# Optimization experiments

Hardware: AMD Instinct MI355X
Metric: run time of the kernel (lower is better)

## Reference

```python
import jax, jax.numpy as jnp
import numpy as np

IN_U = 1024
OUT_U = 1024
BATCH = 4096
HID = 20            # ceil(log2(IN_U*OUT_U)), layer_encoding_dim=0 since num_layers=1
MLP_H = 10
FEAT = 3 + 3 * HID  # 63


def setup_inputs() -> dict:
    key = jax.random.key(0)
    ks = jax.random.split(key, 6)
    X = jax.random.normal(ks[0], (BATCH, IN_U), dtype=jnp.float32)
    weight = jax.random.normal(ks[1], (IN_U, OUT_U), dtype=jnp.float32) * 0.02
    # binary positional encodings per cell (encode_weight_hidden_states)
    k = jnp.arange(IN_U * OUT_U, dtype=jnp.int32).reshape(IN_U, OUT_U)
    shifts = jnp.arange(HID - 1, -1, -1, dtype=jnp.int32)
    hidden = ((k[..., None] >> shifts) & 1).astype(jnp.float32)  # [IN_U, OUT_U, HID]
    W1 = jax.random.normal(ks[2], (FEAT, MLP_H), dtype=jnp.float32) / np.float32(np.sqrt(FEAT))
    b1 = jnp.zeros((MLP_H,), jnp.float32)
    W2 = jax.random.normal(ks[3], (MLP_H, MLP_H), dtype=jnp.float32) / np.float32(np.sqrt(MLP_H))
    b2 = jnp.zeros((MLP_H,), jnp.float32)
    W3 = jax.random.normal(ks[4], (MLP_H, 1 + HID), dtype=jnp.float32) / np.float32(np.sqrt(MLP_H))
    b3 = jnp.zeros((1 + HID,), jnp.float32)
    return {"X": X, "weight": weight, "hidden": hidden,
            "W1": W1, "b1": b1, "W2": W2, "b2": b2, "W3": W3, "b3": b3}


def reference(X, weight, hidden, W1, b1, W2, b2, W3, b3):
    n, m = weight.shape
    # exclude-self column means ('forward') and row means ('backward')
    fwd_mean = (jnp.sum(weight, axis=0, keepdims=True) - weight) / (n - 1)   # [n,m]
    bwd_mean = (jnp.sum(weight, axis=1, keepdims=True) - weight) / (m - 1)   # [n,m]
    fwd_hs = (jnp.sum(hidden, axis=0, keepdims=True) - hidden) / (n - 1)     # [n,m,H]
    bwd_hs = (jnp.sum(hidden, axis=1, keepdims=True) - hidden) / (m - 1)     # [n,m,H]
    feat = jnp.concatenate(
        [weight[..., None], fwd_mean[..., None], bwd_mean[..., None],
         hidden, fwd_hs, bwd_hs], axis=-1)                                   # [n,m,3+3H]
    h = jax.nn.relu(jnp.einsum('nmf,fh->nmh', feat, W1) + b1)
    h = jax.nn.relu(jnp.einsum('nmh,hk->nmk', h, W2) + b2)
    updates = jnp.einsum('nmk,ko->nmo', h, W3) + b3                          # [n,m,1+H]
    new_weight = weight + updates[..., 0]
    # (hidden states also get updates[...,1:] in the torch module, but only the
    #  softmax output is returned)
    logits = jax.nn.relu(X @ new_weight)                                     # [B,m]
    return jax.nn.softmax(logits, axis=-1)
```

## Files before the change

### kernel.cpp

```cpp
#include <hip/hip_runtime.h>
#include <hip/hip_bf16.h>
#include <stdint.h>


#define RS_OFF      0
#define CSPART_OFF  4096
#define BT_OFF      266240
#define AH_OFF      2363392
#define CH_OFF      10752000

typedef __attribute__((ext_vector_type(8))) _Float16 f16x8;
typedef __attribute__((ext_vector_type(4))) float f32x4;

__device__ __forceinline__ unsigned short f2h(float x) {
    _Float16 h = (_Float16)x;
    unsigned short u;
    __builtin_memcpy(&u, &h, 2);
    return u;
}
__device__ __forceinline__ float h2f(unsigned short u) {
    _Float16 h;
    __builtin_memcpy(&h, &u, 2);
    return (float)h;
}
__device__ __forceinline__ void gld16(const void* g, void* l) {
    __builtin_amdgcn_global_load_lds(
        (const __attribute__((address_space(1))) unsigned*)g,
        (__attribute__((address_space(3))) unsigned*)l, 16, 0, 0);
}

__global__ __launch_bounds__(256) void k_pre(const float* __restrict__ w,
        float* __restrict__ rs, float* __restrict__ cs_part) {
    __shared__ float part[4][1024];
    int t = threadIdx.x;
    int lane = t & 63, wv = t >> 6;
    int r0 = blockIdx.x * 16 + wv * 4;
    float ccol[16];
    #pragma unroll
    for (int j = 0; j < 16; ++j) ccol[j] = 0.f;
    #pragma unroll
    for (int rr = 0; rr < 4; ++rr) {
        int row = r0 + rr;
        float rsum = 0.f;
        #pragma unroll
        for (int j = 0; j < 16; ++j) {
            float v = w[(size_t)row * 1024 + j * 64 + lane];
            ccol[j] += v;
            rsum += v;
        }
        #pragma unroll
        for (int o = 32; o; o >>= 1) rsum += __shfl_down(rsum, o);
        if (lane == 0) rs[row] = rsum;
    }
    #pragma unroll
    for (int j = 0; j < 16; ++j) part[wv][j * 64 + lane] = ccol[j];
    __syncthreads();
    #pragma unroll
    for (int j = 0; j < 4; ++j) {
        int c = t + j * 256;
        cs_part[(size_t)blockIdx.x * 1024 + c] =
            part[0][c] + part[1][c] + part[2][c] + part[3][c];
    }
}

__global__ __launch_bounds__(256) void k_nw(const float* __restrict__ w,
        const float* __restrict__ X,
        const float* __restrict__ rs, const float* __restrict__ cs_part,
        const float* __restrict__ W1, const float* __restrict__ b1,
        const float* __restrict__ W2, const float* __restrict__ b2,
        const float* __restrict__ W3, const float* __restrict__ b3,
        unsigned short* __restrict__ Bt, unsigned short* __restrict__ Ah) {
    __shared__ float sW1[630], sW2[100], sb1[10], sb2[10], sw3[10], sa[10];
    __shared__ float rs_loc[32], cs_loc[32];
    __shared__ float rn_loc[320], cm_loc[320];
    __shared__ float st[32][33];
    int t = threadIdx.x;
    if (blockIdx.x >= 1024) {
        int b2x = blockIdx.x - 1024;
        int rb = (b2x & 7) * 512 + (b2x >> 3) * 4;
        size_t rbase = (size_t)rb * 1024;
        #pragma unroll
        for (int p = 0; p < 4; ++p) {
            size_t idx = rbase + p * 1024 + t * 4;
            float4 v = *(const float4*)&X[idx];
            ushort4 h;
            h.x = f2h(v.x); h.y = f2h(v.y); h.z = f2h(v.z); h.w = f2h(v.w);
            *(ushort4*)&Ah[idx] = h;
        }
        return;
    }
    int n0 = (blockIdx.x & 31) * 32;
    int m0 = (blockIdx.x >> 5) * 32;
    const float inv = 1.0f / 1023.0f;

    for (int i = t; i < 630; i += 256) sW1[i] = W1[i];
    if (t < 100) sW2[t] = W2[t];
    if (t >= 128 && t < 138) { sb1[t - 128] = b1[t - 128]; sb2[t - 128] = b2[t - 128]; }
    if (t >= 160 && t < 170) sw3[t - 160] = W3[(t - 160) * 21];
    if (t >= 192 && t < 224) rs_loc[t - 192] = rs[n0 + t - 192];
    if (t >= 224 && t < 256) {
        float s = 0.f;
        #pragma unroll
        for (int p = 0; p < 64; ++p) s += cs_part[(size_t)p * 1024 + m0 + (t - 224)];
        cs_loc[t - 224] = s;
    }
    float b30 = b3[0];
    __syncthreads();
    if (t < 10) sa[t] = sW1[t] - (sW1[10 + t] + sW1[20 + t]) * inv;
    for (int id = t; id < 640; id += 256) {
        int h = id % 10, i = (id / 10) & 31, side = id >= 320;
        if (!side) {
            int n = n0 + i;
            float v = rs_loc[i] * sW1[20 + h] * inv;
            #pragma unroll
            for (int j = 0; j < 10; j++) {
                float bit = (float)((n >> (9 - j)) & 1);
                v += bit * (sW1[(3 + j) * 10 + h] + sW1[(43 + j) * 10 + h]
                            - sW1[(23 + j) * 10 + h] * inv);
                v += (512.0f * inv) * sW1[(23 + j) * 10 + h];
            }
            rn_loc[i * 10 + h] = v;
        } else {
            int m = m0 + i;
            float v = cs_loc[i] * sW1[10 + h] * inv + sb1[h];
            #pragma unroll
            for (int j = 0; j < 10; j++) {
                float bit = (float)((m >> (9 - j)) & 1);
                v += bit * (sW1[(13 + j) * 10 + h] + sW1[(33 + j) * 10 + h]
                            - sW1[(53 + j) * 10 + h] * inv);
                v += (512.0f * inv) * sW1[(53 + j) * 10 + h];
            }
            cm_loc[i * 10 + h] = v;
        }
    }
    __syncthreads();
    int ml = t & 31;
    #pragma unroll
    for (int i = 0; i < 4; i++) {
        int nl = (t >> 5) + 8 * i;
        float wv = w[(size_t)(n0 + nl) * 1024 + m0 + ml];
        float h1[10];
        #pragma unroll
        for (int h = 0; h < 10; h++)
            h1[h] = fmaxf(wv * sa[h] + rn_loc[nl * 10 + h] + cm_loc[ml * 10 + h], 0.f);
        float u = b30;
        #pragma unroll
        for (int k = 0; k < 10; k++) {
            float h2 = sb2[k];
            #pragma unroll
            for (int h = 0; h < 10; h++) h2 += h1[h] * sW2[h * 10 + k];
            u += fmaxf(h2, 0.f) * sw3[k];
        }
        st[nl][ml] = wv + u;
    }
    __syncthreads();
    int mrow = t >> 3, kc = t & 7;
    unsigned short hi4[4];
    #pragma unroll
    for (int j = 0; j < 4; j++)
        hi4[j] = f2h(st[kc * 4 + j][mrow]);
    size_t base = (size_t)(m0 + mrow) * 1024 + n0 + kc * 4;
    *(ushort4*)&Bt[base] = make_ushort4(hi4[0], hi4[1], hi4[2], hi4[3]);
}

__global__ __launch_bounds__(256, 3) void k_gemm13(const unsigned short* __restrict__ Ah,
        const unsigned short* __restrict__ Bt, unsigned short* __restrict__ Ch) {
    __shared__ unsigned short sAh[128 * 64];
    __shared__ unsigned short sBh[64 * 64];
    int tid = threadIdx.x;
    int lane = tid & 63, w = tid >> 6;
    int b = blockIdx.x;
    int xcd = b & 7, s = b >> 3;
    int ty = (xcd << 2) | (s >> 4);
    int tx = s & 15;
    int n0 = tx * 64, m0 = ty * 128;
    int wm = (w >> 1) * 64, wn = (w & 1) * 32;
    int quad = lane >> 4, l16 = lane & 15;

    f32x4 acc[4][2];
    #pragma unroll
    for (int i = 0; i < 4; i++)
        #pragma unroll
        for (int j = 0; j < 2; j++) acc[i][j] = (f32x4)0.f;

    for (int it = 0; it < 16; ++it) {
        int kb = it * 64;
        __syncthreads();
        #pragma unroll
        for (int s2 = 0; s2 < 4; ++s2) {
            int P = s2 * 256 + tid;
            int row = P >> 3;
            int seg = (P & 7) ^ (row & 7);
            int ldsOff = (s2 * 256 + w * 64) * 8;
            size_t ga = (size_t)(m0 + row) * 1024 + kb + seg * 8;
            gld16(&Ah[ga], &sAh[ldsOff]);
        }
        #pragma unroll
        for (int s2 = 0; s2 < 2; ++s2) {
            int P = s2 * 256 + tid;
            int row = P >> 3;
            int seg = (P & 7) ^ (row & 7);
            int ldsOff = (s2 * 256 + w * 64) * 8;
            size_t gb = (size_t)(n0 + row) * 1024 + kb + seg * 8;
            gld16(&Bt[gb], &sBh[ldsOff]);
        }
        __syncthreads();
        #pragma unroll
        for (int ks = 0; ks < 2; ++ks) {
            int segk = ks * 4 + quad;
            f16x8 ah[4], bh[2];
            #pragma unroll
            for (int i = 0; i < 4; ++i) {
                int ra = wm + i * 16 + l16;
                int ca = (ra * 8 + (segk ^ (ra & 7))) * 8;
                ah[i] = *(const f16x8*)&sAh[ca];
            }
            #pragma unroll
            for (int j = 0; j < 2; ++j) {
                int rb = wn + j * 16 + l16;
                int cb = (rb * 8 + (segk ^ (rb & 7))) * 8;
                bh[j] = *(const f16x8*)&sBh[cb];
            }
            #pragma unroll
            for (int i = 0; i < 4; ++i)
                #pragma unroll
                for (int j = 0; j < 2; ++j)
                    acc[i][j] = __builtin_amdgcn_mfma_f32_16x16x32_f16(ah[i], bh[j], acc[i][j], 0, 0, 0);
        }
    }
    #pragma unroll
    for (int i = 0; i < 4; ++i) {
        int mr = m0 + wm + i * 16 + quad * 4;
        #pragma unroll
        for (int j = 0; j < 2; ++j) {
            int nc = n0 + wn + j * 16 + l16;
            #pragma unroll
            for (int r = 0; r < 4; ++r)
                Ch[(size_t)(mr + r) * 1024 + nc] = f2h(fmaxf(acc[i][j][r], 0.f));
        }
    }
}

__global__ __launch_bounds__(256) void k_softmax3(const unsigned short* __restrict__ Ch,
        float* __restrict__ out) {
    int b = blockIdx.x;
    int row = (b & 7) * 512 + (b >> 3);
    int t = threadIdx.x, lane = t & 63, wv = t >> 6;
    __shared__ float red[8];
    ushort4 hv = *(const ushort4*)&Ch[(size_t)row * 1024 + t * 4];
    float4 v;
    v.x = h2f(hv.x); v.y = h2f(hv.y); v.z = h2f(hv.z); v.w = h2f(hv.w);
    float lm = fmaxf(fmaxf(v.x, v.y), fmaxf(v.z, v.w));
    #pragma unroll
    for (int o = 32; o; o >>= 1) lm = fmaxf(lm, __shfl_down(lm, o));
    if (lane == 0) red[wv] = lm;
    __syncthreads();
    float mx = fmaxf(fmaxf(red[0], red[1]), fmaxf(red[2], red[3]));
    float4 e;
    e.x = __expf(v.x - mx); e.y = __expf(v.y - mx);
    e.z = __expf(v.z - mx); e.w = __expf(v.w - mx);
    float ls = e.x + e.y + e.z + e.w;
    #pragma unroll
    for (int o = 32; o; o >>= 1) ls += __shfl_down(ls, o);
    if (lane == 0) red[4 + wv] = ls;
    __syncthreads();
    float inv = 1.0f / (red[4] + red[5] + red[6] + red[7]);
    e.x *= inv; e.y *= inv; e.z *= inv; e.w *= inv;
    *(float4*)&out[(size_t)row * 1024 + t * 4] = e;
}

extern "C" void kernel_launch(void* const* d_in, const int* in_sizes, int n_in,
                              void* d_out, int out_size, void* d_ws, size_t ws_size,
                              hipStream_t stream) {
    const float* X  = (const float*)d_in[0];
    const float* W  = (const float*)d_in[1];
    const float* W1 = (const float*)d_in[3];
    const float* b1 = (const float*)d_in[4];
    const float* W2 = (const float*)d_in[5];
    const float* b2 = (const float*)d_in[6];
    const float* W3 = (const float*)d_in[7];
    const float* b3 = (const float*)d_in[8];

    char* wsb = (char*)d_ws;
    float* rs            = (float*)(wsb + RS_OFF);
    float* cs_part       = (float*)(wsb + CSPART_OFF);
    unsigned short* Bt   = (unsigned short*)(wsb + BT_OFF);
    unsigned short* Ah   = (unsigned short*)(wsb + AH_OFF);
    unsigned short* Ch   = (unsigned short*)(wsb + CH_OFF);
    float* out = (float*)d_out;

    k_pre<<<64, 256, 0, stream>>>(W, rs, cs_part);
    k_nw<<<2048, 256, 0, stream>>>(W, X, rs, cs_part, W1, b1, W2, b2, W3, b3, Bt, Ah);
    k_gemm13<<<512, 256, 0, stream>>>(Ah, Bt, Ch);
    k_softmax3<<<4096, 256, 0, stream>>>(Ch, out);
}
```

Before: 175.1 us.

## Fuse X fp32-to-fp16 conversion into GEMM with register prefetch

Removes the separate conversion pass that wrote a half-precision copy of X to workspace inside k_nw. The GEMM now reads fp32 X directly, converts it in registers and stores it to LDS, with a register prefetch of the next K tile to overlap the global loads. This avoids writing and rereading an 8 MB intermediate. In exchange the A loads become synchronous register loads of twice the bytes, re-read by each of the 16 column-tile blocks, and register pressure rises under the 3-waves launch bound.

```diff
diff --git a/kernel.cpp b/kernel.cpp
--- a/kernel.cpp
+++ b/kernel.cpp
@@ -6,7 +6,6 @@
 #define RS_OFF      0
 #define CSPART_OFF  4096
 #define BT_OFF      266240
-#define AH_OFF      2363392
 #define CH_OFF      10752000
 
 typedef __attribute__((ext_vector_type(8))) _Float16 f16x8;
@@ -64,31 +63,16 @@
 }
 
 __global__ __launch_bounds__(256) void k_nw(const float* __restrict__ w,
-        const float* __restrict__ X,
         const float* __restrict__ rs, const float* __restrict__ cs_part,
         const float* __restrict__ W1, const float* __restrict__ b1,
         const float* __restrict__ W2, const float* __restrict__ b2,
         const float* __restrict__ W3, const float* __restrict__ b3,
-        unsigned short* __restrict__ Bt, unsigned short* __restrict__ Ah) {
+        unsigned short* __restrict__ Bt) {
     __shared__ float sW1[630], sW2[100], sb1[10], sb2[10], sw3[10], sa[10];
     __shared__ float rs_loc[32], cs_loc[32];
     __shared__ float rn_loc[320], cm_loc[320];
     __shared__ float st[32][33];
     int t = threadIdx.x;
-    if (blockIdx.x >= 1024) {
-        int b2x = blockIdx.x - 1024;
-        int rb = (b2x & 7) * 512 + (b2x >> 3) * 4;
-        size_t rbase = (size_t)rb * 1024;
-        #pragma unroll
-        for (int p = 0; p < 4; ++p) {
-            size_t idx = rbase + p * 1024 + t * 4;
-            float4 v = *(const float4*)&X[idx];
-            ushort4 h;
-            h.x = f2h(v.x); h.y = f2h(v.y); h.z = f2h(v.z); h.w = f2h(v.w);
-            *(ushort4*)&Ah[idx] = h;
-        }
-        return;
-    }
     int n0 = (blockIdx.x & 31) * 32;
     int m0 = (blockIdx.x >> 5) * 32;
     const float inv = 1.0f / 1023.0f;
@@ -163,7 +147,7 @@
     *(ushort4*)&Bt[base] = make_ushort4(hi4[0], hi4[1], hi4[2], hi4[3]);
 }
 
-__global__ __launch_bounds__(256, 3) void k_gemm13(const unsigned short* __restrict__ Ah,
+__global__ __launch_bounds__(256, 3) void k_gemm14(const float* __restrict__ X,
         const unsigned short* __restrict__ Bt, unsigned short* __restrict__ Ch) {
     __shared__ unsigned short sAh[128 * 64];
     __shared__ unsigned short sBh[64 * 64];
@@ -183,17 +167,35 @@
         #pragma unroll
         for (int j = 0; j < 2; j++) acc[i][j] = (f32x4)0.f;
 
+    int rowA[4], segA[4];
+    #pragma unroll
+    for (int s2 = 0; s2 < 4; ++s2) {
+        int P = s2 * 256 + tid;
+        rowA[s2] = P >> 3;
+        segA[s2] = (P & 7) ^ (rowA[s2] & 7);
+    }
+
+    float4 pf0[4], pf1[4];
+    #pragma unroll
+    for (int s2 = 0; s2 < 4; ++s2) {
+        const float* ga = &X[(size_t)(m0 + rowA[s2]) * 1024 + segA[s2] * 8];
+        pf0[s2] = *(const float4*)(ga);
+        pf1[s2] = *(const float4*)(ga + 4);
+    }
+
     for (int it = 0; it < 16; ++it) {
         int kb = it * 64;
         __syncthreads();
         #pragma unroll
         for (int s2 = 0; s2 < 4; ++s2) {
             int P = s2 * 256 + tid;
-            int row = P >> 3;
-            int seg = (P & 7) ^ (row & 7);
-            int ldsOff = (s2 * 256 + w * 64) * 8;
-            size_t ga = (size_t)(m0 + row) * 1024 + kb + seg * 8;
-            gld16(&Ah[ga], &sAh[ldsOff]);
+            float4 a0 = pf0[s2], a1 = pf1[s2];
+            f16x8 hv;
+            hv[0] = (_Float16)a0.x; hv[1] = (_Float16)a0.y;
+            hv[2] = (_Float16)a0.z; hv[3] = (_Float16)a0.w;
+            hv[4] = (_Float16)a1.x; hv[5] = (_Float16)a1.y;
+            hv[6] = (_Float16)a1.z; hv[7] = (_Float16)a1.w;
+            *(f16x8*)&sAh[P * 8] = hv;
         }
         #pragma unroll
         for (int s2 = 0; s2 < 2; ++s2) {
@@ -203,6 +205,15 @@
             int ldsOff = (s2 * 256 + w * 64) * 8;
             size_t gb = (size_t)(n0 + row) * 1024 + kb + seg * 8;
             gld16(&Bt[gb], &sBh[ldsOff]);
+        }
+        if (it < 15) {
+            int kb2 = kb + 64;
+            #pragma unroll
+            for (int s2 = 0; s2 < 4; ++s2) {
+                const float* ga = &X[(size_t)(m0 + rowA[s2]) * 1024 + kb2 + segA[s2] * 8];
+                pf0[s2] = *(const float4*)(ga);
+                pf1[s2] = *(const float4*)(ga + 4);
+            }
         }
         __syncthreads();
         #pragma unroll
@@ -285,12 +296,11 @@
     float* rs            = (float*)(wsb + RS_OFF);
     float* cs_part       = (float*)(wsb + CSPART_OFF);
     unsigned short* Bt   = (unsigned short*)(wsb + BT_OFF);
-    unsigned short* Ah   = (unsigned short*)(wsb + AH_OFF);
     unsigned short* Ch   = (unsigned short*)(wsb + CH_OFF);
     float* out = (float*)d_out;
 
     k_pre<<<64, 256, 0, stream>>>(W, rs, cs_part);
-    k_nw<<<2048, 256, 0, stream>>>(W, X, rs, cs_part, W1, b1, W2, b2, W3, b3, Bt, Ah);
-    k_gemm13<<<512, 256, 0, stream>>>(Ah, Bt, Ch);
+    k_nw<<<1024, 256, 0, stream>>>(W, rs, cs_part, W1, b1, W2, b2, W3, b3, Bt);
+    k_gemm14<<<512, 256, 0, stream>>>(X, Bt, Ch);
     k_softmax3<<<4096, 256, 0, stream>>>(Ch, out);
 }
```

Measured after the change: 184.9 us. +5.6%, slower.
